# Performance work log

Hardware: AMD Instinct MI355X
Metric: run time of the kernel (lower is better)

## Reference

```python
import jax, jax.numpy as jnp
import numpy as np

GROUPS = 4  # init kwarg


def setup_inputs() -> dict:
    key = jax.random.key(0)
    k1, k2, k3, k4 = jax.random.split(key, 4)
    B, S, D, H = 4, 4096, 256, 10
    # 0.02 scale on weights keeps unscaled QK^T logits in a sane range
    # (original torch code uses raw randn weights and applies NO 1/sqrt(d)
    # scaling inside group_attention, which saturates softmax).
    return {
        "x": jax.random.normal(k1, (B, S, D), dtype=jnp.float32),
        "Wq": jax.random.normal(k2, (H, D, D), dtype=jnp.float32) * 0.02,
        "Wk": jax.random.normal(k3, (H, D, D), dtype=jnp.float32) * 0.02,
        "Wo": jax.random.normal(k4, (D, H * D), dtype=jnp.float32) * 0.02,
    }


def reference(x, Wq, Wk, Wo):
    # x: [B,S,D]; Wq/Wk: [H,D,D]; Wo: [D, H*D] (nn.Linear weight layout)
    H, D, _ = Wq.shape
    B, S, _ = x.shape
    G = GROUPS
    C = S // G  # chunk length

    Q = jnp.einsum('bsd,hde->hbse', x, Wq)  # [H,B,S,D]
    K = jnp.einsum('bsd,hde->hbse', x, Wk)
    # Faithful to source bug: V is projected with wk weights -> V == K

    Qg = Q.reshape(H, B, G, C, D)
    KVg = jnp.roll(K.reshape(H, B, G, C, D), shift=-1, axis=2)  # chunk i attends chunk (i+1)%G

    # NOTE: original applies NO scaling to logits (scale arg unused)
    S_ = jnp.einsum('hbgqd,hbgkd->hbgqk', Qg, KVg)   # [H,B,G,C,C]
    P = jax.nn.softmax(S_, axis=-1)
    O = jnp.einsum('hbgqk,hbgkd->hbgqd', P, KVg)     # [H,B,G,C,D]

    # concat heads on feature dim: [B,S,H*D]
    out = O.reshape(H, B, S, D).transpose(1, 2, 0, 3).reshape(B, S, H * D)
    return jnp.einsum('bsk,dk->bsd', out, Wo)  # final Linear (no bias)
```

## Files before the change

kernel.cpp:

```cpp
#include <hip/hip_runtime.h>

typedef float f32x4 __attribute__((ext_vector_type(4)));
typedef short s16x8 __attribute__((ext_vector_type(8)));
typedef unsigned int u32;

#define BSZ 4
#define SEQ 4096
#define DIM 256
#define NH 10
#define NG 4
#define CHK 1024
#define BS_TOT 16384
#define HD 2560

__device__ __forceinline__ unsigned short f2bf(float f) {
    unsigned int u = __builtin_bit_cast(unsigned int, f);
    u = (u + 0x7fffu + ((u >> 16) & 1u)) >> 16;
    return (unsigned short)u;
}

__device__ __forceinline__ void gload_lds16(const unsigned short* g, unsigned short* l) {
    __builtin_amdgcn_global_load_lds((const __attribute__((address_space(1))) u32*)g,
                                     (__attribute__((address_space(3))) u32*)l, 16, 0, 0);
}


__global__ __launch_bounds__(256) void cast_f32_bf16(const float* __restrict__ s,
                                                     unsigned short* __restrict__ d, int n) {
    long i = 4L * (blockIdx.x * 256 + threadIdx.x);
    if (i < n) {
        float4 v = *(const float4*)(s + i);
        ushort4 o;
        o.x = f2bf(v.x); o.y = f2bf(v.y); o.z = f2bf(v.z); o.w = f2bf(v.w);
        *(ushort4*)(d + i) = o;
    }
}

__global__ __launch_bounds__(256) void transpose_cast_w(const float* __restrict__ Wq,
                                                        const float* __restrict__ Wk,
                                                        unsigned short* __restrict__ wqt,
                                                        unsigned short* __restrict__ wkt) {
    const float* W = (blockIdx.z & 1) ? Wk : Wq;
    unsigned short* Wt = (blockIdx.z & 1) ? wkt : wqt;
    int h = blockIdx.z >> 1;
    __shared__ float tile[32][33];
    int d0 = blockIdx.x * 32, e0 = blockIdx.y * 32;
    int tx = threadIdx.x & 31, ty = threadIdx.x >> 5;
    const float* Wh = W + (long)h * 65536;
    unsigned short* Wth = Wt + (long)h * 65536;
#pragma unroll
    for (int r = ty; r < 32; r += 8) tile[r][tx] = Wh[(long)(d0 + r) * 256 + e0 + tx];
    __syncthreads();
#pragma unroll
    for (int r = ty; r < 32; r += 8) Wth[(long)(e0 + r) * 256 + d0 + tx] = f2bf(tile[tx][r]);
}


__device__ __forceinline__ void gemm_body(const unsigned short* __restrict__ A, long lda,
                                          const unsigned short* __restrict__ Bt, long ldb,
                                          unsigned short* Cb, float* Cf, long ldc,
                                          int K, bool accum, long mbase,
                                          unsigned short* KTo) {
    __shared__ unsigned short As[64 * 40];
    __shared__ unsigned short Bs[256 * 40];
    const int t = threadIdx.x;
    const int w = t >> 6, l = t & 63, lr = l & 15, lg = l >> 4;

    f32x4 acc[16];
#pragma unroll
    for (int i = 0; i < 16; i++) acc[i] = (f32x4){0.f, 0.f, 0.f, 0.f};

    const int ar = t >> 2, akc = (t & 3) * 8;

    for (int k0 = 0; k0 < K; k0 += 32) {
        *(s16x8*)(&As[ar * 40 + akc]) = *(const s16x8*)(A + (mbase + ar) * lda + k0 + akc);
#pragma unroll
        for (int s = 0; s < 4; s++) {
            int n = s * 64 + (t >> 2);
            *(s16x8*)(&Bs[n * 40 + akc]) = *(const s16x8*)(Bt + (long)n * ldb + k0 + akc);
        }
        __syncthreads();
        s16x8 af = *(const s16x8*)(&As[(w * 16 + lr) * 40 + lg * 8]);
        __builtin_amdgcn_s_setprio(1);
#pragma unroll
        for (int nt = 0; nt < 16; nt++) {
            s16x8 bf = *(const s16x8*)(&Bs[(nt * 16 + lr) * 40 + lg * 8]);
            acc[nt] = __builtin_amdgcn_mfma_f32_16x16x32_bf16(af, bf, acc[nt], 0, 0, 0);
        }
        __builtin_amdgcn_s_setprio(0);
        __syncthreads();
    }
    long m0 = mbase + w * 16 + lg * 4;
#pragma unroll
    for (int nt = 0; nt < 16; nt++) {
        int col = nt * 16 + lr;
#pragma unroll
        for (int r = 0; r < 4; r++) {
            long idx = (m0 + r) * ldc + col;
            if (Cb) {
                Cb[idx] = f2bf(acc[nt][r]);
            } else {
                float v = acc[nt][r];
                if (accum) v += Cf[idx];
                Cf[idx] = v;
            }
        }
    }
    if (KTo) {
        int bg = (int)(m0 >> 10);
        int key0 = (int)(m0 & 1023);
        unsigned short* base = KTo + (long)bg * (256 * 1024)
                             + (long)(key0 >> 5) * (256 * 32) + (key0 & 31);
#pragma unroll
        for (int nt = 0; nt < 16; nt++) {
            int col = nt * 16 + lr;
            ushort4 v;
            v.x = f2bf(acc[nt][0]); v.y = f2bf(acc[nt][1]);
            v.z = f2bf(acc[nt][2]); v.w = f2bf(acc[nt][3]);
            *(ushort4*)(base + (long)col * 32) = v;
        }
    }
}

__global__ __launch_bounds__(256) void proj_kernel(const unsigned short* __restrict__ xb,
                                                   const unsigned short* __restrict__ wqt,
                                                   const unsigned short* __restrict__ wkt,
                                                   unsigned short* Qb, unsigned short* Kb,
                                                   unsigned short* KTb,
                                                   int h0, long headStrideOut, long headStrideKT) {
    int h = h0 + blockIdx.y;
    bool isK = (blockIdx.z != 0);
    const unsigned short* Bt = (isK ? wkt : wqt) + (long)h * 65536;
    unsigned short* C = (isK ? Kb : Qb) + (long)blockIdx.y * headStrideOut;
    unsigned short* KTo = isK ? (KTb + (long)blockIdx.y * headStrideKT) : nullptr;
    gemm_body(xb, 256, Bt, 256, C, nullptr, 256, 256, false, (long)blockIdx.x * 64, KTo);
}

__global__ __launch_bounds__(256) void final_kernel(const unsigned short* __restrict__ Ob, long lda,
                                                    const unsigned short* __restrict__ wob, long ldb,
                                                    float* out, int K, int accum) {
    gemm_body(Ob, lda, wob, ldb, nullptr, out, 256, K, accum != 0, (long)blockIdx.x * 64, nullptr);
}


__global__ __launch_bounds__(256, 3) void proj128(const unsigned short* __restrict__ xb,
                                                  const unsigned short* __restrict__ wqt,
                                                  const unsigned short* __restrict__ wkt,
                                                  unsigned short* __restrict__ Qb,
                                                  unsigned short* __restrict__ Kb,
                                                  unsigned short* __restrict__ KTb,
                                                  long headStrideOut, long headStrideKT) {
    __shared__ unsigned short As[2][128 * 32];
    __shared__ unsigned short Bs[2][128 * 32];

    const int lb = blockIdx.x;
    const int logical = (lb & 7) * 640 + (lb >> 3);
    const int x = logical / 40;
    const int u = logical - x * 40;
    const int mat = u >> 1, ntile = u & 1;
    const int h = mat >> 1;
    const bool isK = (mat & 1) != 0;

    const unsigned short* A = xb;
    const unsigned short* Bt = (isK ? wkt : wqt) + (long)h * 65536 + (long)ntile * 128 * 256;
    unsigned short* C = (isK ? Kb : Qb) + (long)h * headStrideOut;
    unsigned short* KTo = isK ? (KTb + (long)h * headStrideKT) : nullptr;
    const long mbase = (long)x * 128;
    const int ncol0 = ntile * 128;

    const int t = threadIdx.x, w = t >> 6, l = t & 63, lr = l & 15, lg = l >> 4;
    const int wm = w >> 1, wn = w & 1;

    int sOff[2];
#pragma unroll
    for (int i = 0; i < 2; i++) {
        int row = w * 32 + i * 16 + (l >> 2);
        int cs = (l & 3) ^ (row & 3);
        sOff[i] = row * 256 + cs * 8;
    }

    f32x4 acc[4][4];
#pragma unroll
    for (int i = 0; i < 4; i++)
#pragma unroll
        for (int j = 0; j < 4; j++) acc[i][j] = (f32x4){0.f, 0.f, 0.f, 0.f};

#define PSTAGE(buf, k0) do {                                                     \
        _Pragma("unroll")                                                        \
        for (int i = 0; i < 2; i++)                                              \
            gload_lds16(A + mbase * 256 + (k0) + sOff[i],                        \
                        &As[buf][(w * 32 + i * 16) * 32]);                       \
        _Pragma("unroll")                                                        \
        for (int i = 0; i < 2; i++)                                              \
            gload_lds16(Bt + (k0) + sOff[i],                                     \
                        &Bs[buf][(w * 32 + i * 16) * 32]);                       \
    } while (0)

    PSTAGE(0, 0);
    __syncthreads();
    int cur = 0;
    for (int ks = 0; ks < 8; ++ks) {
        if (ks < 7) PSTAGE(cur ^ 1, (ks + 1) * 32);
        s16x8 a[4], b[4];
#pragma unroll
        for (int mf = 0; mf < 4; mf++) {
            int row = wm * 64 + mf * 16 + lr;
            a[mf] = *(const s16x8*)(&As[cur][row * 32 + (lg ^ (row & 3)) * 8]);
        }
#pragma unroll
        for (int nf = 0; nf < 4; nf++) {
            int row = wn * 64 + nf * 16 + lr;
            b[nf] = *(const s16x8*)(&Bs[cur][row * 32 + (lg ^ (row & 3)) * 8]);
        }
        __builtin_amdgcn_s_setprio(1);
#pragma unroll
        for (int mf = 0; mf < 4; mf++)
#pragma unroll
            for (int nf = 0; nf < 4; nf++)
                acc[mf][nf] = __builtin_amdgcn_mfma_f32_16x16x32_bf16(a[mf], b[nf], acc[mf][nf], 0, 0, 0);
        __builtin_amdgcn_s_setprio(0);
        __syncthreads();
        cur ^= 1;
    }
#undef PSTAGE

    long m0 = mbase + wm * 64 + lg * 4;
#pragma unroll
    for (int mf = 0; mf < 4; mf++) {
        long mrow = m0 + mf * 16;
#pragma unroll
        for (int nf = 0; nf < 4; nf++) {
            int col = ncol0 + wn * 64 + nf * 16 + lr;
#pragma unroll
            for (int r = 0; r < 4; r++) C[(mrow + r) * 256 + col] = f2bf(acc[mf][nf][r]);
        }
    }
    if (KTo) {
#pragma unroll
        for (int mf = 0; mf < 4; mf++) {
            long key = m0 + mf * 16;
            int bg = (int)(key >> 10), k0i = (int)(key & 1023);
            unsigned short* base = KTo + (long)bg * (256 * 1024)
                                 + (long)(k0i >> 5) * (256 * 32) + (k0i & 31);
#pragma unroll
            for (int nf = 0; nf < 4; nf++) {
                int col = ncol0 + wn * 64 + nf * 16 + lr;
                ushort4 v;
                v.x = f2bf(acc[mf][nf][0]); v.y = f2bf(acc[mf][nf][1]);
                v.z = f2bf(acc[mf][nf][2]); v.w = f2bf(acc[mf][nf][3]);
                *(ushort4*)(base + (long)col * 32) = v;
            }
        }
    }
}


__global__ __launch_bounds__(256, 3) void final128(const unsigned short* __restrict__ Ob,
                                                   long headStride,
                                                   const unsigned short* __restrict__ wob,
                                                   float* __restrict__ out) {
    __shared__ unsigned short As[2][128 * 32];
    __shared__ unsigned short Bs[2][128 * 32];

    const int lb = blockIdx.x;
    const int logical = (lb & 7) * 32 + (lb >> 3);
    const int x = logical >> 1, ntile = logical & 1;
    const long mbase = (long)x * 128;
    const int ncol0 = ntile * 128;
    const unsigned short* Bt = wob + (long)ncol0 * HD;

    const int t = threadIdx.x, w = t >> 6, l = t & 63, lr = l & 15, lg = l >> 4;
    const int wm = w >> 1, wn = w & 1;

    int sOffA[2], sOffB[2];
#pragma unroll
    for (int i = 0; i < 2; i++) {
        int row = w * 32 + i * 16 + (l >> 2);
        int cs = (l & 3) ^ (row & 3);
        sOffA[i] = row * 256 + cs * 8;
        sOffB[i] = row * HD + cs * 8;
    }

    f32x4 acc[4][4];
#pragma unroll
    for (int i = 0; i < 4; i++)
#pragma unroll
        for (int j = 0; j < 4; j++) acc[i][j] = (f32x4){0.f, 0.f, 0.f, 0.f};

#define FSTAGE(buf, k0) do {                                                     \
        const unsigned short* Asrc = Ob + (long)((k0) >> 8) * headStride         \
                                   + mbase * 256 + ((k0) & 255);                 \
        _Pragma("unroll")                                                        \
        for (int i = 0; i < 2; i++)                                              \
            gload_lds16(Asrc + sOffA[i], &As[buf][(w * 32 + i * 16) * 32]);      \
        _Pragma("unroll")                                                        \
        for (int i = 0; i < 2; i++)                                              \
            gload_lds16(Bt + (k0) + sOffB[i], &Bs[buf][(w * 32 + i * 16) * 32]); \
    } while (0)

    FSTAGE(0, 0);
    __syncthreads();
    int cur = 0;
    for (int ks = 0; ks < 80; ++ks) {
        if (ks < 79) FSTAGE(cur ^ 1, (ks + 1) * 32);
        s16x8 a[4], b[4];
#pragma unroll
        for (int mf = 0; mf < 4; mf++) {
            int row = wm * 64 + mf * 16 + lr;
            a[mf] = *(const s16x8*)(&As[cur][row * 32 + (lg ^ (row & 3)) * 8]);
        }
#pragma unroll
        for (int nf = 0; nf < 4; nf++) {
            int row = wn * 64 + nf * 16 + lr;
            b[nf] = *(const s16x8*)(&Bs[cur][row * 32 + (lg ^ (row & 3)) * 8]);
        }
        __builtin_amdgcn_s_setprio(1);
#pragma unroll
        for (int mf = 0; mf < 4; mf++)
#pragma unroll
            for (int nf = 0; nf < 4; nf++)
                acc[mf][nf] = __builtin_amdgcn_mfma_f32_16x16x32_bf16(a[mf], b[nf], acc[mf][nf], 0, 0, 0);
        __builtin_amdgcn_s_setprio(0);
        __syncthreads();
        cur ^= 1;
    }
#undef FSTAGE

    long m0 = mbase + wm * 64 + lg * 4;
#pragma unroll
    for (int mf = 0; mf < 4; mf++) {
        long mrow = m0 + mf * 16;
#pragma unroll
        for (int nf = 0; nf < 4; nf++) {
            int col = ncol0 + wn * 64 + nf * 16 + lr;
#pragma unroll
            for (int r = 0; r < 4; r++) out[(mrow + r) * 256 + col] = acc[mf][nf][r];
        }
    }
}


__global__ __launch_bounds__(256, 2) void attn_kernel(const unsigned short* __restrict__ Qb,
                                                      const unsigned short* __restrict__ Kb,
                                                      long headStrideQK,
                                                      const unsigned short* __restrict__ KTg,
                                                      long headStrideKT,
                                                      unsigned short* __restrict__ Ob,
                                                      long ldo, long colStride,
                                                      int chunkPerXcd) {
    const int lb = blockIdx.x;
    const int logical = (lb & 7) * chunkPerXcd + (lb >> 3);
    const int bx = logical & 7;
    const int by = (logical >> 3) & 15;
    const int h = logical >> 7;

    const unsigned short* Q = Qb + (long)h * headStrideQK;
    const unsigned short* Kp = Kb + (long)h * headStrideQK;
    const unsigned short* KT = KTg + (long)h * headStrideKT;
    unsigned short* O = Ob + (long)h * colStride;
    const int b = by >> 2, g = by & 3;
    const long qrow0 = (long)b * SEQ + (long)g * CHK + (long)bx * 128;
    const long krow0 = (long)b * SEQ + (long)((g + 1) & 3) * CHK;
    const unsigned short* KTc = KT + (long)(b * NG + ((g + 1) & 3)) * (256 * 1024);

    __shared__ unsigned short Krm[2][32 * 256];
    __shared__ unsigned short KTt[2][256 * 32];

    const int t = threadIdx.x;
    const int w = t >> 6, l = t & 63, lr = l & 15, lg = l >> 4;

    s16x8 qf[2][8];
#pragma unroll
    for (int qh = 0; qh < 2; qh++) {
        const unsigned short* qp = Q + (qrow0 + w * 32 + qh * 16 + lr) * 256 + lg * 8;
#pragma unroll
        for (int s = 0; s < 8; s++) qf[qh][s] = *(const s16x8*)(qp + s * 32);
    }

    f32x4 o[2][16];
#pragma unroll
    for (int qh = 0; qh < 2; qh++)
#pragma unroll
        for (int i = 0; i < 16; i++) o[qh][i] = (f32x4){0.f, 0.f, 0.f, 0.f};
    float l_part[2] = {0.f, 0.f};

    int kOff[4], tOff[4];
#pragma unroll
    for (int i = 0; i < 4; i++) {
        int rowK = w * 8 + i * 2 + (l >> 5);
        kOff[i] = rowK * 256 + (((l & 31) ^ (rowK & 7)) * 8);
        int rowT = w * 64 + i * 16 + (l >> 2);
        tOff[i] = rowT * 32 + (((l & 3) ^ ((rowT >> 1) & 3)) * 8);
    }

#define STAGE(buf, kt_) do {                                                    \
        const unsigned short* Ksrc = Kp + (krow0 + (long)(kt_) * 32) * 256;     \
        const unsigned short* Tsrc = KTc + (long)(kt_) * (32 * 256);            \
        _Pragma("unroll")                                                       \
        for (int i = 0; i < 4; i++)                                             \
            gload_lds16(Ksrc + kOff[i], &Krm[buf][(w * 8 + i * 2) * 256]);      \
        _Pragma("unroll")                                                       \
        for (int i = 0; i < 4; i++)                                             \
            gload_lds16(Tsrc + tOff[i], &KTt[buf][(w * 64 + i * 16) * 32]);     \
    } while (0)

    STAGE(0, 0);
    __syncthreads();
    int cur = 0;

    for (int kt = 0; kt < 32; ++kt) {
        if (kt < 31) STAGE(cur ^ 1, kt + 1);

        f32x4 st00 = (f32x4){0.f, 0.f, 0.f, 0.f}, st01 = st00, st10 = st00, st11 = st00;
        __builtin_amdgcn_s_setprio(1);
#pragma unroll
        for (int s = 0; s < 8; s++) {
            int c0 = ((s * 4 + lg) ^ (lr & 7)) * 8;
            s16x8 a0 = *(const s16x8*)(&Krm[cur][lr * 256 + c0]);
            s16x8 a1 = *(const s16x8*)(&Krm[cur][(16 + lr) * 256 + c0]);
            st00 = __builtin_amdgcn_mfma_f32_16x16x32_bf16(a0, qf[0][s], st00, 0, 0, 0);
            st01 = __builtin_amdgcn_mfma_f32_16x16x32_bf16(a1, qf[0][s], st01, 0, 0, 0);
            st10 = __builtin_amdgcn_mfma_f32_16x16x32_bf16(a0, qf[1][s], st10, 0, 0, 0);
            st11 = __builtin_amdgcn_mfma_f32_16x16x32_bf16(a1, qf[1][s], st11, 0, 0, 0);
        }
        __builtin_amdgcn_s_setprio(0);

        s16x8 pa[2];
#pragma unroll
        for (int qh = 0; qh < 2; qh++) {
            f32x4 s0 = qh ? st10 : st00, s1 = qh ? st11 : st01;
            float p0 = __expf(s0[0]), p1 = __expf(s0[1]), p2 = __expf(s0[2]), p3 = __expf(s0[3]);
            float p4 = __expf(s1[0]), p5 = __expf(s1[1]), p6 = __expf(s1[2]), p7 = __expf(s1[3]);
            l_part[qh] += ((p0 + p1) + (p2 + p3)) + ((p4 + p5) + (p6 + p7));
            unsigned int u00 = (unsigned)f2bf(p0) | ((unsigned)f2bf(p1) << 16);
            unsigned int u01 = (unsigned)f2bf(p2) | ((unsigned)f2bf(p3) << 16);
            unsigned int u10 = (unsigned)f2bf(p4) | ((unsigned)f2bf(p5) << 16);
            unsigned int u11 = (unsigned)f2bf(p6) | ((unsigned)f2bf(p7) << 16);
            int sA = ((2 * lg) & 3) * 16 + lr;
            int sB = ((2 * lg + 1) & 3) * 16 + lr;
            unsigned int w0a = __shfl(u00, sA), w0b = __shfl(u10, sA);
            unsigned int w1a = __shfl(u01, sA), w1b = __shfl(u11, sA);
            unsigned int w2a = __shfl(u00, sB), w2b = __shfl(u10, sB);
            unsigned int w3a = __shfl(u01, sB), w3b = __shfl(u11, sB);
            bool hi = (lg >> 1) != 0;
            unsigned int aw0 = hi ? w0b : w0a, aw1 = hi ? w1b : w1a;
            unsigned int aw2 = hi ? w2b : w2a, aw3 = hi ? w3b : w3a;
            struct { unsigned int a, b, c, d; } awx = {aw0, aw1, aw2, aw3};
            pa[qh] = __builtin_bit_cast(s16x8, awx);
        }

        __builtin_amdgcn_s_setprio(1);
#pragma unroll
        for (int nt = 0; nt < 16; nt++) {
            int d = nt * 16 + lr;
            int c = (lg ^ ((d >> 1) & 3)) * 8;
            s16x8 bv = *(const s16x8*)(&KTt[cur][d * 32 + c]);
            o[0][nt] = __builtin_amdgcn_mfma_f32_16x16x32_bf16(pa[0], bv, o[0][nt], 0, 0, 0);
            o[1][nt] = __builtin_amdgcn_mfma_f32_16x16x32_bf16(pa[1], bv, o[1][nt], 0, 0, 0);
        }
        __builtin_amdgcn_s_setprio(0);

        __syncthreads();
        cur ^= 1;
    }
#undef STAGE

#pragma unroll
    for (int qh = 0; qh < 2; qh++) {
        float lt = l_part[qh] + __shfl_xor(l_part[qh], 16);
        lt += __shfl_xor(lt, 32);
        float rinv = 1.0f / lt;
        float ri[4];
#pragma unroll
        for (int r = 0; r < 4; r++) ri[r] = __shfl(rinv, lg * 4 + r);
        long orow0 = qrow0 + w * 32 + qh * 16 + lg * 4;
#pragma unroll
        for (int nt = 0; nt < 16; nt++) {
#pragma unroll
            for (int r = 0; r < 4; r++) {
                O[(orow0 + r) * ldo + nt * 16 + lr] = f2bf(o[qh][nt][r] * ri[r]);
            }
        }
    }
}


extern "C" void kernel_launch(void* const* d_in, const int* in_sizes, int n_in,
                              void* d_out, int out_size, void* d_ws, size_t ws_size,
                              hipStream_t stream) {
    const float* x  = (const float*)d_in[0];
    const float* Wq = (const float*)d_in[1];
    const float* Wk = (const float*)d_in[2];
    const float* Wo = (const float*)d_in[3];
    float* out = (float*)d_out;
    char* ws = (char*)d_ws;

    unsigned short* xb  = (unsigned short*)(ws);
    unsigned short* wqt = (unsigned short*)(ws + 8388608);
    unsigned short* wkt = (unsigned short*)(ws + 9699328);
    unsigned short* wob = (unsigned short*)(ws + 11010048);
    char* dyn = ws + 12320768;

    cast_f32_bf16<<<4096, 256, 0, stream>>>(x, xb, BS_TOT * DIM);
    cast_f32_bf16<<<640, 256, 0, stream>>>(Wo, wob, DIM * HD);
    transpose_cast_w<<<dim3(8, 8, 2 * NH), 256, 0, stream>>>(Wq, Wk, wqt, wkt);

    const long perHeadElems = (long)BS_TOT * DIM;
    const size_t FULL_NEED = 12320768ULL + 3ULL * 83886080ULL;

    if (ws_size >= FULL_NEED) {
        unsigned short* Qb  = (unsigned short*)dyn;
        unsigned short* Kb  = Qb + (long)NH * perHeadElems;
        unsigned short* KTb = Kb + (long)NH * perHeadElems;
        proj128<<<5120, 256, 0, stream>>>(xb, wqt, wkt, Qb, Kb, KTb,
                                          perHeadElems, perHeadElems);
        attn_kernel<<<1280, 256, 0, stream>>>(Qb, Kb, perHeadElems, KTb, perHeadElems,
                                              Qb, 256, perHeadElems, 160);
        final128<<<256, 256, 0, stream>>>(Qb, perHeadElems, wob, out);
    } else {
        unsigned short* Qh  = (unsigned short*)dyn;
        unsigned short* Kh  = Qh + perHeadElems;
        unsigned short* KTh = Kh + perHeadElems;
        hipMemsetAsync(d_out, 0, (size_t)out_size * 4, stream);
        for (int h = 0; h < NH; ++h) {
            proj_kernel<<<dim3(256, 1, 2), 256, 0, stream>>>(xb, wqt, wkt, Qh, Kh, KTh, h, 0, 0);
            attn_kernel<<<128, 256, 0, stream>>>(Qh, Kh, 0, KTh, 0, Qh, 256, 0, 16);
            final_kernel<<<256, 256, 0, stream>>>(Qh, 256, wob + h * 256, HD, out, 256, 1);
        }
    }
}
```

Baseline: 358.8 us.

## Switch attention to 32x32x16 MFMA with exp2 prescale and permlane swaps

The attention kernel now uses 32x32x16 bf16 MFMAs instead of 16x16x32 tiles for both QK^T and PV. Each wave covers its 32 query rows with a single accumulator tile for the scores and eight tiles for the output. Q is prescaled by log2(e) in the projection kernels so the softmax can use the native exp2. Probabilities are packed with v_cvt_pk_bf16_f32, and the P operand is rearranged with v_permlane32_swap instead of many shuffles. The aim is to cut MFMA issue count, transcendental cost and cross-lane shuffle overhead, with the risk of changed register pressure and a layout mismatch in the output mapping.

```diff
diff --git a/kernel.cpp b/kernel.cpp
--- a/kernel.cpp
+++ b/kernel.cpp
@@ -1,6 +1,7 @@
 #include <hip/hip_runtime.h>
 
 typedef float f32x4 __attribute__((ext_vector_type(4)));
+typedef float f32x16 __attribute__((ext_vector_type(16)));
 typedef short s16x8 __attribute__((ext_vector_type(8)));
 typedef unsigned int u32;
 
@@ -12,6 +13,7 @@
 #define CHK 1024
 #define BS_TOT 16384
 #define HD 2560
+#define LOG2E 1.44269504f
 
 __device__ __forceinline__ unsigned short f2bf(float f) {
     unsigned int u = __builtin_bit_cast(unsigned int, f);
@@ -22,6 +24,12 @@
 __device__ __forceinline__ void gload_lds16(const unsigned short* g, unsigned short* l) {
     __builtin_amdgcn_global_load_lds((const __attribute__((address_space(1))) u32*)g,
                                      (__attribute__((address_space(3))) u32*)l, 16, 0, 0);
+}
+
+__device__ __forceinline__ u32 cvtpk_bf16(float lo, float hi) {
+    u32 r;
+    asm("v_cvt_pk_bf16_f32 %0, %1, %2" : "=v"(r) : "v"(lo), "v"(hi));
+    return r;
 }
 
 
@@ -60,7 +68,7 @@
                                           const unsigned short* __restrict__ Bt, long ldb,
                                           unsigned short* Cb, float* Cf, long ldc,
                                           int K, bool accum, long mbase,
-                                          unsigned short* KTo) {
+                                          unsigned short* KTo, float cscale) {
     __shared__ unsigned short As[64 * 40];
     __shared__ unsigned short Bs[256 * 40];
     const int t = threadIdx.x;
@@ -98,7 +106,7 @@
         for (int r = 0; r < 4; r++) {
             long idx = (m0 + r) * ldc + col;
             if (Cb) {
-                Cb[idx] = f2bf(acc[nt][r]);
+                Cb[idx] = f2bf(acc[nt][r] * cscale);
             } else {
                 float v = acc[nt][r];
                 if (accum) v += Cf[idx];
@@ -133,13 +141,15 @@
     const unsigned short* Bt = (isK ? wkt : wqt) + (long)h * 65536;
     unsigned short* C = (isK ? Kb : Qb) + (long)blockIdx.y * headStrideOut;
     unsigned short* KTo = isK ? (KTb + (long)blockIdx.y * headStrideKT) : nullptr;
-    gemm_body(xb, 256, Bt, 256, C, nullptr, 256, 256, false, (long)blockIdx.x * 64, KTo);
+    gemm_body(xb, 256, Bt, 256, C, nullptr, 256, 256, false, (long)blockIdx.x * 64, KTo,
+              isK ? 1.0f : LOG2E);
 }
 
 __global__ __launch_bounds__(256) void final_kernel(const unsigned short* __restrict__ Ob, long lda,
                                                     const unsigned short* __restrict__ wob, long ldb,
                                                     float* out, int K, int accum) {
-    gemm_body(Ob, lda, wob, ldb, nullptr, out, 256, K, accum != 0, (long)blockIdx.x * 64, nullptr);
+    gemm_body(Ob, lda, wob, ldb, nullptr, out, 256, K, accum != 0, (long)blockIdx.x * 64,
+              nullptr, 1.0f);
 }
 
 
@@ -160,6 +170,7 @@
     const int mat = u >> 1, ntile = u & 1;
     const int h = mat >> 1;
     const bool isK = (mat & 1) != 0;
+    const float cs = isK ? 1.0f : LOG2E;
 
     const unsigned short* A = xb;
     const unsigned short* Bt = (isK ? wkt : wqt) + (long)h * 65536 + (long)ntile * 128 * 256;
@@ -175,8 +186,8 @@
 #pragma unroll
     for (int i = 0; i < 2; i++) {
         int row = w * 32 + i * 16 + (l >> 2);
-        int cs = (l & 3) ^ (row & 3);
-        sOff[i] = row * 256 + cs * 8;
+        int cs2 = (l & 3) ^ (row & 3);
+        sOff[i] = row * 256 + cs2 * 8;
     }
 
     f32x4 acc[4][4];
@@ -232,7 +243,7 @@
         for (int nf = 0; nf < 4; nf++) {
             int col = ncol0 + wn * 64 + nf * 16 + lr;
 #pragma unroll
-            for (int r = 0; r < 4; r++) C[(mrow + r) * 256 + col] = f2bf(acc[mf][nf][r]);
+            for (int r = 0; r < 4; r++) C[(mrow + r) * 256 + col] = f2bf(acc[mf][nf][r] * cs);
         }
     }
     if (KTo) {
@@ -276,9 +287,9 @@
 #pragma unroll
     for (int i = 0; i < 2; i++) {
         int row = w * 32 + i * 16 + (l >> 2);
-        int cs = (l & 3) ^ (row & 3);
-        sOffA[i] = row * 256 + cs * 8;
-        sOffB[i] = row * HD + cs * 8;
+        int cs2 = (l & 3) ^ (row & 3);
+        sOffA[i] = row * 256 + cs2 * 8;
+        sOffB[i] = row * HD + cs2 * 8;
     }
 
     f32x4 acc[4][4];
@@ -367,22 +378,21 @@
     __shared__ unsigned short KTt[2][256 * 32];
 
     const int t = threadIdx.x;
-    const int w = t >> 6, l = t & 63, lr = l & 15, lg = l >> 4;
-
-    s16x8 qf[2][8];
-#pragma unroll
-    for (int qh = 0; qh < 2; qh++) {
-        const unsigned short* qp = Q + (qrow0 + w * 32 + qh * 16 + lr) * 256 + lg * 8;
-#pragma unroll
-        for (int s = 0; s < 8; s++) qf[qh][s] = *(const s16x8*)(qp + s * 32);
-    }
-
-    f32x4 o[2][16];
-#pragma unroll
-    for (int qh = 0; qh < 2; qh++)
-#pragma unroll
-        for (int i = 0; i < 16; i++) o[qh][i] = (f32x4){0.f, 0.f, 0.f, 0.f};
-    float l_part[2] = {0.f, 0.f};
+    const int w = t >> 6, l = t & 63, l31 = l & 31, hi = l >> 5;
+
+    s16x8 qf[16];
+    {
+        const unsigned short* qp = Q + (qrow0 + w * 32 + l31) * 256 + hi * 8;
+#pragma unroll
+        for (int s = 0; s < 16; s++) qf[s] = *(const s16x8*)(qp + s * 16);
+    }
+
+    f32x16 o[8];
+#pragma unroll
+    for (int i = 0; i < 8; i++)
+#pragma unroll
+        for (int j = 0; j < 16; j++) o[i][j] = 0.f;
+    float l_part = 0.f;
 
     int kOff[4], tOff[4];
 #pragma unroll
@@ -411,52 +421,55 @@
     for (int kt = 0; kt < 32; ++kt) {
         if (kt < 31) STAGE(cur ^ 1, kt + 1);
 
-        f32x4 st00 = (f32x4){0.f, 0.f, 0.f, 0.f}, st01 = st00, st10 = st00, st11 = st00;
+        f32x16 st;
+#pragma unroll
+        for (int j = 0; j < 16; j++) st[j] = 0.f;
         __builtin_amdgcn_s_setprio(1);
 #pragma unroll
-        for (int s = 0; s < 8; s++) {
-            int c0 = ((s * 4 + lg) ^ (lr & 7)) * 8;
-            s16x8 a0 = *(const s16x8*)(&Krm[cur][lr * 256 + c0]);
-            s16x8 a1 = *(const s16x8*)(&Krm[cur][(16 + lr) * 256 + c0]);
-            st00 = __builtin_amdgcn_mfma_f32_16x16x32_bf16(a0, qf[0][s], st00, 0, 0, 0);
-            st01 = __builtin_amdgcn_mfma_f32_16x16x32_bf16(a1, qf[0][s], st01, 0, 0, 0);
-            st10 = __builtin_amdgcn_mfma_f32_16x16x32_bf16(a0, qf[1][s], st10, 0, 0, 0);
-            st11 = __builtin_amdgcn_mfma_f32_16x16x32_bf16(a1, qf[1][s], st11, 0, 0, 0);
+        for (int ks = 0; ks < 16; ks++) {
+            int col = ((2 * ks + hi) ^ (l31 & 7)) * 8;
+            s16x8 kf = *(const s16x8*)(&Krm[cur][l31 * 256 + col]);
+            st = __builtin_amdgcn_mfma_f32_32x32x16_bf16(kf, qf[ks], st, 0, 0, 0);
         }
         __builtin_amdgcn_s_setprio(0);
 
-        s16x8 pa[2];
-#pragma unroll
-        for (int qh = 0; qh < 2; qh++) {
-            f32x4 s0 = qh ? st10 : st00, s1 = qh ? st11 : st01;
-            float p0 = __expf(s0[0]), p1 = __expf(s0[1]), p2 = __expf(s0[2]), p3 = __expf(s0[3]);
-            float p4 = __expf(s1[0]), p5 = __expf(s1[1]), p6 = __expf(s1[2]), p7 = __expf(s1[3]);
-            l_part[qh] += ((p0 + p1) + (p2 + p3)) + ((p4 + p5) + (p6 + p7));
-            unsigned int u00 = (unsigned)f2bf(p0) | ((unsigned)f2bf(p1) << 16);
-            unsigned int u01 = (unsigned)f2bf(p2) | ((unsigned)f2bf(p3) << 16);
-            unsigned int u10 = (unsigned)f2bf(p4) | ((unsigned)f2bf(p5) << 16);
-            unsigned int u11 = (unsigned)f2bf(p6) | ((unsigned)f2bf(p7) << 16);
-            int sA = ((2 * lg) & 3) * 16 + lr;
-            int sB = ((2 * lg + 1) & 3) * 16 + lr;
-            unsigned int w0a = __shfl(u00, sA), w0b = __shfl(u10, sA);
-            unsigned int w1a = __shfl(u01, sA), w1b = __shfl(u11, sA);
-            unsigned int w2a = __shfl(u00, sB), w2b = __shfl(u10, sB);
-            unsigned int w3a = __shfl(u01, sB), w3b = __shfl(u11, sB);
-            bool hi = (lg >> 1) != 0;
-            unsigned int aw0 = hi ? w0b : w0a, aw1 = hi ? w1b : w1a;
-            unsigned int aw2 = hi ? w2b : w2a, aw3 = hi ? w3b : w3a;
-            struct { unsigned int a, b, c, d; } awx = {aw0, aw1, aw2, aw3};
-            pa[qh] = __builtin_bit_cast(s16x8, awx);
-        }
+        u32 c0, c1, c2, c3, c4, c5, c6, c7;
+        {
+            float pa0 = __builtin_amdgcn_exp2f(st[0]),  pa1 = __builtin_amdgcn_exp2f(st[1]);
+            float pa2 = __builtin_amdgcn_exp2f(st[2]),  pa3 = __builtin_amdgcn_exp2f(st[3]);
+            float pa4 = __builtin_amdgcn_exp2f(st[4]),  pa5 = __builtin_amdgcn_exp2f(st[5]);
+            float pa6 = __builtin_amdgcn_exp2f(st[6]),  pa7 = __builtin_amdgcn_exp2f(st[7]);
+            float pa8 = __builtin_amdgcn_exp2f(st[8]),  pa9 = __builtin_amdgcn_exp2f(st[9]);
+            float paA = __builtin_amdgcn_exp2f(st[10]), paB = __builtin_amdgcn_exp2f(st[11]);
+            float paC = __builtin_amdgcn_exp2f(st[12]), paD = __builtin_amdgcn_exp2f(st[13]);
+            float paE = __builtin_amdgcn_exp2f(st[14]), paF = __builtin_amdgcn_exp2f(st[15]);
+            l_part += (((pa0 + pa1) + (pa2 + pa3)) + ((pa4 + pa5) + (pa6 + pa7)))
+                    + (((pa8 + pa9) + (paA + paB)) + ((paC + paD) + (paE + paF)));
+            c0 = cvtpk_bf16(pa0, pa1); c1 = cvtpk_bf16(pa2, pa3);
+            c2 = cvtpk_bf16(pa4, pa5); c3 = cvtpk_bf16(pa6, pa7);
+            c4 = cvtpk_bf16(pa8, pa9); c5 = cvtpk_bf16(paA, paB);
+            c6 = cvtpk_bf16(paC, paD); c7 = cvtpk_bf16(paE, paF);
+        }
+        asm("v_permlane32_swap_b32 %0, %1" : "+v"(c0), "+v"(c2));
+        asm("v_permlane32_swap_b32 %0, %1" : "+v"(c1), "+v"(c3));
+        asm("v_permlane32_swap_b32 %0, %1" : "+v"(c4), "+v"(c6));
+        asm("v_permlane32_swap_b32 %0, %1" : "+v"(c5), "+v"(c7));
+        struct { u32 a, b, c, d; } x0 = {c0, c1, c2, c3};
+        struct { u32 a, b, c, d; } x1 = {c4, c5, c6, c7};
+        s16x8 pa0f = __builtin_bit_cast(s16x8, x0);
+        s16x8 pa1f = __builtin_bit_cast(s16x8, x1);
 
         __builtin_amdgcn_s_setprio(1);
 #pragma unroll
-        for (int nt = 0; nt < 16; nt++) {
-            int d = nt * 16 + lr;
-            int c = (lg ^ ((d >> 1) & 3)) * 8;
-            s16x8 bv = *(const s16x8*)(&KTt[cur][d * 32 + c]);
-            o[0][nt] = __builtin_amdgcn_mfma_f32_16x16x32_bf16(pa[0], bv, o[0][nt], 0, 0, 0);
-            o[1][nt] = __builtin_amdgcn_mfma_f32_16x16x32_bf16(pa[1], bv, o[1][nt], 0, 0, 0);
+        for (int ks = 0; ks < 2; ks++) {
+            s16x8 paf = ks ? pa1f : pa0f;
+#pragma unroll
+            for (int nt = 0; nt < 8; nt++) {
+                int d = nt * 32 + l31;
+                int col = ((2 * ks + hi) ^ ((d >> 1) & 3)) * 8;
+                s16x8 bv = *(const s16x8*)(&KTt[cur][d * 32 + col]);
+                o[nt] = __builtin_amdgcn_mfma_f32_32x32x16_bf16(paf, bv, o[nt], 0, 0, 0);
+            }
         }
         __builtin_amdgcn_s_setprio(0);
 
@@ -465,21 +478,20 @@
     }
 #undef STAGE
 
-#pragma unroll
-    for (int qh = 0; qh < 2; qh++) {
-        float lt = l_part[qh] + __shfl_xor(l_part[qh], 16);
-        lt += __shfl_xor(lt, 32);
-        float rinv = 1.0f / lt;
-        float ri[4];
-#pragma unroll
-        for (int r = 0; r < 4; r++) ri[r] = __shfl(rinv, lg * 4 + r);
-        long orow0 = qrow0 + w * 32 + qh * 16 + lg * 4;
-#pragma unroll
-        for (int nt = 0; nt < 16; nt++) {
-#pragma unroll
-            for (int r = 0; r < 4; r++) {
-                O[(orow0 + r) * ldo + nt * 16 + lr] = f2bf(o[qh][nt][r] * ri[r]);
-            }
+    float lt = l_part + __shfl_xor(l_part, 32);
+    float rinv = 1.0f / lt;
+    float ri[16];
+#pragma unroll
+    for (int reg = 0; reg < 16; reg++) {
+        int qr = (reg & 3) + 8 * (reg >> 2) + 4 * hi;
+        ri[reg] = __shfl(rinv, qr);
+    }
+#pragma unroll
+    for (int nt = 0; nt < 8; nt++) {
+#pragma unroll
+        for (int reg = 0; reg < 16; reg++) {
+            int qr = (reg & 3) + 8 * (reg >> 2) + 4 * hi;
+            O[(qrow0 + w * 32 + qr) * ldo + nt * 32 + l31] = f2bf(o[nt][reg] * ri[reg]);
         }
     }
 }
```

After: 347.1 us. -3.3%, faster.
